# Kernel optimization log

Hardware: AMD Instinct MI355X
Metric: run time of the kernel (lower is better)

Reference implementation:

```python
import jax, jax.numpy as jnp
import numpy as np
from jax import lax

NIMG = 4          # num_image_channels (dx for these is zeroed each step)
C = 64            # total channels = 4 + 44 + 16
NFILT = 2         # learned depthwise filters
HID = 256         # hidden_size
FIRE = 0.5        # fire_rate
B, H, W = 16, 128, 128
STEPS = 8


def setup_inputs() -> dict:
    key = jax.random.key(0)
    ks = jax.random.split(key, 7)
    x = jax.random.normal(ks[0], (B, H, W, C), jnp.float32)
    # depthwise 3x3 kernels, OIHW with I=1 (groups = C)
    w_conv1 = jax.random.normal(ks[1], (C, 1, 3, 3), jnp.float32) * 0.3
    w_conv2 = jax.random.normal(ks[2], (C, 1, 3, 3), jnp.float32) * 0.3
    fan_in = C * (NFILT + 1)  # 192
    w_hidden = jax.random.normal(ks[3], (HID, fan_in), jnp.float32) / np.sqrt(fan_in).astype(np.float32)
    b_hidden = jax.random.normal(ks[4], (HID,), jnp.float32) * 0.01
    # original zero-inits final_layer; use small random weights for a nontrivial baseline
    w_final = jax.random.normal(ks[5], (C, HID), jnp.float32) * 0.02
    rand_vals = jax.random.uniform(ks[6], (STEPS, B, H, W, 1), jnp.float32)
    return {"x": x, "w_conv1": w_conv1, "w_conv2": w_conv2,
            "w_hidden": w_hidden, "b_hidden": b_hidden, "w_final": w_final,
            "rand_vals": rand_vals, "steps": STEPS}


def _dwconv(xc, w):
    # xc: [B, C, W, H]; reflect-pad then valid depthwise 3x3 (groups=C)
    xp = jnp.pad(xc, ((0, 0), (0, 0), (1, 1), (1, 1)), mode='reflect')
    return lax.conv_general_dilated(xp, w, (1, 1), 'VALID',
                                    dimension_numbers=('NCHW', 'OIHW', 'NCHW'),
                                    feature_group_count=C)


def reference(x, w_conv1, w_conv2, w_hidden, b_hidden, w_final, rand_vals, steps):
    dtype = x.dtype
    ch_mask = (jnp.arange(C) >= NIMG).astype(dtype)  # zero image-channel updates

    def step(xc, rnd):
        # xc: [B, C, W, H]  (torch layout after x.transpose(1,3))
        y = jnp.concatenate([xc, _dwconv(xc, w_conv1), _dwconv(xc, w_conv2)], axis=1)  # [B,3C,W,H]
        yt = jnp.transpose(y, (0, 3, 2, 1))  # [B,H,W,3C]
        h = jax.nn.relu(jnp.einsum('bhwf,of->bhwo', yt, w_hidden) + b_hidden)
        dx = jnp.einsum('bhwo,co->bhwc', h, w_final)  # [B,H,W,C]
        dx = dx * (rnd > FIRE).astype(dtype) * ch_mask  # stochastic gate + immutable image channels
        xc = xc + jnp.transpose(dx, (0, 3, 2, 1))
        life = (xc[:, 0:1] > 0).astype(dtype)  # channel-0 life mask broadcast over channels
        return xc * life, None

    xc0 = jnp.transpose(x, (0, 3, 2, 1))  # NHWC -> [B,C,W,H]
    xcN, _ = lax.scan(step, xc0, rand_vals)
    return jnp.transpose(xcN, (0, 3, 2, 1))  # back to NHWC
```

## Files before the change

kernel.cpp:

```cpp
#include <hip/hip_runtime.h>

#define BB 16
#define HH 128
#define WW 128
#define CH 64
#define TPX 64
#define NTH 512
#define NPIX (BB*HH*WW)
#define KF 192
#define HID 256

#define WS_WTP 0u
#define WS_WFP 98304u
#define WS_WCB 131072u
#define WS_ST  135680u

typedef __attribute__((ext_vector_type(8))) short short8;
typedef __attribute__((ext_vector_type(8))) unsigned short ushort8;
typedef __attribute__((ext_vector_type(4))) float f4;

#define OFF_WCV 25344
#define OFF_FC  32768
#define OFF_LG  49152
#define SMEM_SZ 49664

#define GLDS16(gp, lp) __builtin_amdgcn_global_load_lds( \
    (const __attribute__((address_space(1))) unsigned int*)(gp), \
    (__attribute__((address_space(3))) unsigned int*)(lp), 16, 0, 0)

__device__ __forceinline__ unsigned short f2b(float f) {
    unsigned x = __float_as_uint(f);
    x += 0x7fffu + ((x >> 16) & 1u);
    return (unsigned short)(x >> 16);
}
__device__ __forceinline__ float b2f(unsigned short u) {
    return __uint_as_float(((unsigned)u) << 16);
}
__device__ __forceinline__ int refl(int i, int n) {
    if (i < 0) return -i;
    if (i >= n) return 2*n - 2 - i;
    return i;
}
__device__ __forceinline__ int xrow(int row, int chunk) {
    return row*64 + (((chunk ^ row) & 7) << 3);
}

__global__ __launch_bounds__(256) void prep(
    const float* __restrict__ wh, const float* __restrict__ wf,
    unsigned short* __restrict__ wtp, unsigned short* __restrict__ wfp)
{
    int i = blockIdx.x * 256 + threadIdx.x;
    if (i < 6144) {
        const int l = i & 63, r = i >> 6;
        const int ks = r % 6, ti = r / 6;
        const int row = ti*16 + (l & 15);
        const int k0  = ks*32 + (l >> 4)*8;
        ushort8 v;
        #pragma unroll
        for (int j = 0; j < 8; ++j) v[j] = f2b(wh[row*KF + k0 + j]);
        *(ushort8*)&wtp[(size_t)i * 8] = v;
    } else {
        const int g = i - 6144;
        const int l = g & 63, r = g >> 6;
        const int ks2 = r & 7, cq = r >> 3;
        const int c  = cq*16 + (l & 15);
        const int o0 = ks2*32 + (l >> 4)*8;
        ushort8 v;
        #pragma unroll
        for (int j = 0; j < 8; ++j) v[j] = f2b(wf[c*HID + o0 + j]);
        *(ushort8*)&wfp[(size_t)g * 8] = v;
    }
}

__global__ __launch_bounds__(256) void prep2(
    const float* __restrict__ w1, const float* __restrict__ w2,
    float* __restrict__ wcb)
{
    int i = blockIdx.x * 256 + threadIdx.x;
    if (i < 1152) {
        const int f = i / 576, rem = i - f * 576;
        const int t = rem >> 6, c = rem & 63;
        wcb[i] = (f ? w2 : w1)[c*9 + t];
    }
}

template<int SRCF, int DSTF>
__global__ __launch_bounds__(512, 4) void nca_step(
    const float* __restrict__ xinf, const unsigned short* __restrict__ srcb,
    void* __restrict__ dstv,
    const unsigned short* __restrict__ wtp, const unsigned short* __restrict__ wfp,
    const float* __restrict__ wcbg,
    const float* __restrict__ bh, const float* __restrict__ rnd)
{
    __shared__ __align__(16) char smem[SMEM_SZ];
    unsigned short* xs   = (unsigned short*)smem;
    char*           fch  = smem + OFF_FC;
    float*          wcvb = (float*)(smem + OFF_WCV);
    float*          lgs  = (float*)(smem + OFF_LG);

    const int tid = threadIdx.x;
    const int l = tid & 63, wv = tid >> 6;
    const int lr = l & 15, gq = l >> 4;
    const int w0 = blockIdx.x * TPX;
    const int h  = blockIdx.y;
    const int b  = blockIdx.z;
    const int R  = b * HH + h;

    if (SRCF == 1) {
        #pragma unroll
        for (int it = 0; it < 3; ++it) {
            const int g = wv + it*8;
            const int c = g*64 + l;
            const int row = c >> 3, ckp = c & 7;
            const int r3 = row / 66, px = row - r3*66;
            const int ck = ckp ^ (row & 7);
            const int sr = refl(h - 1 + r3, HH);
            const int sc = refl(w0 - 1 + px, WW);
            const unsigned short* gp = srcb + ((((size_t)b*HH + sr)*WW + sc) << 6) + (ck << 3);
            GLDS16(gp, (char*)xs + (size_t)g*1024);
        }
        if (wv == 0 && l < 48) {
            const int c = 1536 + l;
            const int row = c >> 3, ckp = c & 7;
            const int r3 = row / 66, px = row - r3*66;
            const int ck = ckp ^ (row & 7);
            const int sr = refl(h - 1 + r3, HH);
            const int sc = refl(w0 - 1 + px, WW);
            const unsigned short* gp = srcb + ((((size_t)b*HH + sr)*WW + sc) << 6) + (ck << 3);
            GLDS16(gp, (char*)xs + (size_t)24*1024);
        }
    } else {
        const int q = tid & 3;
        for (int s0 = tid >> 2; s0 < 198; s0 += 128) {
            const int r3 = s0 / 66, wi = s0 - r3*66;
            const int sr = refl(h - 1 + r3, HH);
            const int sc = refl(w0 - 1 + wi, WW);
            const size_t pix = ((size_t)b*HH + sr)*WW + sc;
            const float* p = xinf + pix*64 + q*16;
            f4 a0 = *(const f4*)p, a1 = *(const f4*)(p+4);
            f4 a2 = *(const f4*)(p+8), a3 = *(const f4*)(p+12);
            ushort8 o0, o1;
            o0[0]=f2b(a0.x); o0[1]=f2b(a0.y); o0[2]=f2b(a0.z); o0[3]=f2b(a0.w);
            o0[4]=f2b(a1.x); o0[5]=f2b(a1.y); o0[6]=f2b(a1.z); o0[7]=f2b(a1.w);
            o1[0]=f2b(a2.x); o1[1]=f2b(a2.y); o1[2]=f2b(a2.z); o1[3]=f2b(a2.w);
            o1[4]=f2b(a3.x); o1[5]=f2b(a3.y); o1[6]=f2b(a3.z); o1[7]=f2b(a3.w);
            const int row = r3*66 + wi;
            *(ushort8*)(xs + xrow(row, 2*q))     = o0;
            *(ushort8*)(xs + xrow(row, 2*q + 1)) = o1;
        }
    }
    for (int j = tid; j < 288; j += NTH)
        ((f4*)wcvb)[j] = ((const f4*)wcbg)[j];
    if (tid < TPX) {
        const size_t pix = (size_t)R * WW + w0 + tid;
        lgs[TPX + tid] = (rnd[pix] > 0.5f) ? 1.f : 0.f;
        if (SRCF == 0)
            lgs[tid] = (xinf[pix*64] > 0.f) ? 1.f : 0.f;
    }
    __syncthreads();

    if (SRCF == 1 && tid < TPX)
        lgs[tid] = (b2f(xs[xrow(66 + tid + 1, 0)]) > 0.f) ? 1.f : 0.f;

    {
        const int px = tid >> 3, ck = tid & 7, cg = ck * 8;
        float a1[8], a2[8];
        #pragma unroll
        for (int k = 0; k < 8; ++k) { a1[k] = 0.f; a2[k] = 0.f; }
        #pragma unroll
        for (int t = 0; t < 9; ++t) {
            const int i2 = t / 3, j = t - 3*i2;
            const ushort8 xv = *(const ushort8*)(xs + xrow(j*66 + px + i2, ck));
            const float* w1p = wcvb + t*64 + cg;
            const float* w2p = wcvb + 576 + t*64 + cg;
            #pragma unroll
            for (int k = 0; k < 8; ++k) {
                const float xf = b2f(xv[k]);
                a1[k] = fmaf(xf, w1p[k], a1[k]);
                a2[k] = fmaf(xf, w2p[k], a2[k]);
            }
        }
        ushort8 o1v, o2v;
        #pragma unroll
        for (int k = 0; k < 8; ++k) { o1v[k] = f2b(a1[k]); o2v[k] = f2b(a2[k]); }
        const int sw = (px & 7) << 4;
        *(ushort8*)(fch + ((px*256 + cg*2) ^ sw))       = o1v;
        *(ushort8*)(fch + ((px*256 + 128 + cg*2) ^ sw)) = o2v;
    }
    __syncthreads();

    f4 acc[4][2];
    #pragma unroll
    for (int ot = 0; ot < 2; ++ot) {
        const float bv = bh[wv*32 + ot*16 + lr];
        const f4 bvv = {bv, bv, bv, bv};
        #pragma unroll
        for (int mt = 0; mt < 4; ++mt) acc[mt][ot] = bvv;
    }
    #pragma unroll
    for (int ks = 0; ks < 6; ++ks) {
        short8 afr[4];
        #pragma unroll
        for (int mt = 0; mt < 4; ++mt) {
            const int px = mt*16 + lr;
            if (ks < 2)
                afr[mt] = *(const short8*)(xs + xrow(66 + px + 1, ks*4 + gq));
            else
                afr[mt] = *(const short8*)(fch +
                            ((px*256 + (ks-2)*64 + gq*16) ^ ((px & 7) << 4)));
        }
        #pragma unroll
        for (int ot = 0; ot < 2; ++ot) {
            const short8 bfr = *(const short8*)(wtp + ((((wv*2 + ot)*6 + ks)*64 + l) << 3));
            #pragma unroll
            for (int mt = 0; mt < 4; ++mt)
                acc[mt][ot] = __builtin_amdgcn_mfma_f32_16x16x32_bf16(afr[mt], bfr, acc[mt][ot], 0,0,0);
        }
    }

    const int cq = wv & 3, mh = wv >> 2;
    unsigned short baseb[8];
    #pragma unroll
    for (int mt = 0; mt < 2; ++mt)
      #pragma unroll
      for (int r2 = 0; r2 < 4; ++r2) {
        const int px = mh*32 + mt*16 + gq*4 + r2;
        baseb[mt*4 + r2] = xs[xrow(66 + px + 1, cq*2 + (lr >> 3)) + (lr & 7)];
      }
    __syncthreads();

    #pragma unroll
    for (int mt = 0; mt < 4; ++mt)
      #pragma unroll
      for (int ot = 0; ot < 2; ++ot)
        #pragma unroll
        for (int r2 = 0; r2 < 4; ++r2) {
            const int px = mt*16 + gq*4 + r2;
            const int o  = wv*32 + ot*16 + lr;
            *(unsigned short*)(smem + ((px*512 + o*2) ^ ((px & 7) << 4))) =
                f2b(fmaxf(acc[mt][ot][r2], 0.f));
        }
    __syncthreads();

    f4 acc2[2] = {{0.f,0.f,0.f,0.f},{0.f,0.f,0.f,0.f}};
    #pragma unroll
    for (int ks2 = 0; ks2 < 8; ++ks2) {
        const short8 bw = *(const short8*)(wfp + (((cq*8 + ks2)*64 + l) << 3));
        #pragma unroll
        for (int mt = 0; mt < 2; ++mt) {
            const int px = mh*32 + mt*16 + lr;
            const short8 ha = *(const short8*)(smem + ((px*512 + ks2*64 + gq*16) ^ ((px & 7) << 4)));
            acc2[mt] = __builtin_amdgcn_mfma_f32_16x16x32_bf16(ha, bw, acc2[mt], 0,0,0);
        }
    }

    unsigned short* stageB = (unsigned short*)fch;
    float*          stageF = (float*)fch;
    #pragma unroll
    for (int mt = 0; mt < 2; ++mt)
      #pragma unroll
      for (int r2 = 0; r2 < 4; ++r2) {
        const int px = mh*32 + mt*16 + gq*4 + r2;
        const int c  = cq*16 + lr;
        const float life = lgs[px], g = lgs[TPX + px];
        const float base = b2f(baseb[mt*4 + r2]);
        const float dx   = acc2[mt][r2];
        const float outv = (c >= 4) ? (base + dx * g) * life : base * life;
        if (DSTF == 1) stageF[px*64 + c] = outv;
        else           stageB[px*64 + c] = f2b(outv);
      }
    __syncthreads();

    const size_t pix0 = (size_t)R * WW + w0;
    if (DSTF == 1) {
        float* dstf = (float*)dstv + pix0 * 64;
        for (int i = tid; i < 1024; i += NTH) {
            const f4 v = *(const f4*)(stageF + i*4);
            __builtin_nontemporal_store(v, (f4*)(dstf + i*4));
        }
    } else {
        unsigned short* dstb = (unsigned short*)dstv + pix0 * 64;
        const ushort8 v = *(const ushort8*)(stageB + tid*8);
        __builtin_nontemporal_store(v, (ushort8*)(dstb + tid*8));
    }
}

extern "C" void kernel_launch(void* const* d_in, const int* in_sizes, int n_in,
                              void* d_out, int out_size, void* d_ws, size_t ws_size,
                              hipStream_t stream) {
    const float* xin = (const float*)d_in[0];
    const float* w1  = (const float*)d_in[1];
    const float* w2  = (const float*)d_in[2];
    const float* wh  = (const float*)d_in[3];
    const float* bh  = (const float*)d_in[4];
    const float* wf  = (const float*)d_in[5];
    const float* rv  = (const float*)d_in[6];

    unsigned short* wtp = (unsigned short*)((char*)d_ws + WS_WTP);
    unsigned short* wfp = (unsigned short*)((char*)d_ws + WS_WFP);
    float*          wcb = (float*)((char*)d_ws + WS_WCB);
    unsigned short* stb = (unsigned short*)((char*)d_ws + WS_ST);
    unsigned short* omb = (unsigned short*)d_out;

    prep <<<dim3(32), dim3(256), 0, stream>>>(wh, wf, wtp, wfp);
    prep2<<<dim3(5),  dim3(256), 0, stream>>>(w1, w2, wcb);

    dim3 g(WW / TPX, HH, BB), blk(NTH);
    nca_step<0,0><<<g, blk, 0, stream>>>(xin, nullptr, stb, wtp, wfp, wcb, bh, rv);
    for (int s = 1; s < 7; ++s) {
        const unsigned short* sp = (s & 1) ? stb : omb;
        unsigned short* dp       = (s & 1) ? omb : stb;
        nca_step<1,0><<<g, blk, 0, stream>>>(nullptr, sp, dp, wtp, wfp, wcb, bh,
                                             rv + (size_t)s * NPIX);
    }
    nca_step<1,1><<<g, blk, 0, stream>>>(nullptr, stb, d_out, wtp, wfp, wcb, bh,
                                         rv + (size_t)7 * NPIX);
}
```

Before: 634.0 us.

## Fold depthwise convolutions into hidden-layer weights as a 576-wide MFMA GEMM

Precomputes combined weights W_hidden·conv1/conv2 per 3x3 tap (plus identity at center) so the hidden layer becomes a single K=576 bf16 MFMA GEMM over the 9 shifted neighborhood rows. This removes the scalar FMA depthwise convolution stage, its LDS staging buffer and a barrier. The trade is three times more MFMA work and larger weight fetches from global memory. Precision also shifts, since the fused weights are rounded to bf16 and the conv outputs are never rounded separately.

```diff
diff --git a/kernel.cpp b/kernel.cpp
--- a/kernel.cpp
+++ b/kernel.cpp
@@ -7,20 +7,18 @@
 #define TPX 64
 #define NTH 512
 #define NPIX (BB*HH*WW)
-#define KF 192
+#define KFT 576
 #define HID 256
 
 #define WS_WTP 0u
-#define WS_WFP 98304u
-#define WS_WCB 131072u
-#define WS_ST  135680u
+#define WS_WFP 294912u
+#define WS_ST  327680u
 
 typedef __attribute__((ext_vector_type(8))) short short8;
 typedef __attribute__((ext_vector_type(8))) unsigned short ushort8;
 typedef __attribute__((ext_vector_type(4))) float f4;
 
-#define OFF_WCV 25344
-#define OFF_FC  32768
+#define OFF_STG 32768
 #define OFF_LG  49152
 #define SMEM_SZ 49664
 
@@ -47,20 +45,28 @@
 
 __global__ __launch_bounds__(256) void prep(
     const float* __restrict__ wh, const float* __restrict__ wf,
+    const float* __restrict__ w1, const float* __restrict__ w2,
     unsigned short* __restrict__ wtp, unsigned short* __restrict__ wfp)
 {
     int i = blockIdx.x * 256 + threadIdx.x;
-    if (i < 6144) {
+    if (i < 18432) {
         const int l = i & 63, r = i >> 6;
-        const int ks = r % 6, ti = r / 6;
-        const int row = ti*16 + (l & 15);
-        const int k0  = ks*32 + (l >> 4)*8;
+        const int ks = r % 18, ti = r / 18;
+        const int o  = ti*16 + (l & 15);
+        const int k0 = ks*32 + (l >> 4)*8;
         ushort8 v;
         #pragma unroll
-        for (int j = 0; j < 8; ++j) v[j] = f2b(wh[row*KF + k0 + j]);
+        for (int j = 0; j < 8; ++j) {
+            const int k = k0 + j;
+            const int t = k >> 6, c = k & 63;
+            float val = wh[o*192 + 64 + c]  * w1[c*9 + t]
+                      + wh[o*192 + 128 + c] * w2[c*9 + t];
+            if (t == 4) val += wh[o*192 + c];
+            v[j] = f2b(val);
+        }
         *(ushort8*)&wtp[(size_t)i * 8] = v;
-    } else {
-        const int g = i - 6144;
+    } else if (i < 20480) {
+        const int g = i - 18432;
         const int l = g & 63, r = g >> 6;
         const int ks2 = r & 7, cq = r >> 3;
         const int c  = cq*16 + (l & 15);
@@ -72,31 +78,17 @@
     }
 }
 
-__global__ __launch_bounds__(256) void prep2(
-    const float* __restrict__ w1, const float* __restrict__ w2,
-    float* __restrict__ wcb)
-{
-    int i = blockIdx.x * 256 + threadIdx.x;
-    if (i < 1152) {
-        const int f = i / 576, rem = i - f * 576;
-        const int t = rem >> 6, c = rem & 63;
-        wcb[i] = (f ? w2 : w1)[c*9 + t];
-    }
-}
-
 template<int SRCF, int DSTF>
 __global__ __launch_bounds__(512, 4) void nca_step(
     const float* __restrict__ xinf, const unsigned short* __restrict__ srcb,
     void* __restrict__ dstv,
     const unsigned short* __restrict__ wtp, const unsigned short* __restrict__ wfp,
-    const float* __restrict__ wcbg,
     const float* __restrict__ bh, const float* __restrict__ rnd)
 {
     __shared__ __align__(16) char smem[SMEM_SZ];
-    unsigned short* xs   = (unsigned short*)smem;
-    char*           fch  = smem + OFF_FC;
-    float*          wcvb = (float*)(smem + OFF_WCV);
-    float*          lgs  = (float*)(smem + OFF_LG);
+    unsigned short* xs  = (unsigned short*)smem;
+    char*           stg = smem + OFF_STG;
+    float*          lgs = (float*)(smem + OFF_LG);
 
     const int tid = threadIdx.x;
     const int l = tid & 63, wv = tid >> 6;
@@ -149,8 +141,6 @@
             *(ushort8*)(xs + xrow(row, 2*q + 1)) = o1;
         }
     }
-    for (int j = tid; j < 288; j += NTH)
-        ((f4*)wcvb)[j] = ((const f4*)wcbg)[j];
     if (tid < TPX) {
         const size_t pix = (size_t)R * WW + w0 + tid;
         lgs[TPX + tid] = (rnd[pix] > 0.5f) ? 1.f : 0.f;
@@ -162,33 +152,6 @@
     if (SRCF == 1 && tid < TPX)
         lgs[tid] = (b2f(xs[xrow(66 + tid + 1, 0)]) > 0.f) ? 1.f : 0.f;
 
-    {
-        const int px = tid >> 3, ck = tid & 7, cg = ck * 8;
-        float a1[8], a2[8];
-        #pragma unroll
-        for (int k = 0; k < 8; ++k) { a1[k] = 0.f; a2[k] = 0.f; }
-        #pragma unroll
-        for (int t = 0; t < 9; ++t) {
-            const int i2 = t / 3, j = t - 3*i2;
-            const ushort8 xv = *(const ushort8*)(xs + xrow(j*66 + px + i2, ck));
-            const float* w1p = wcvb + t*64 + cg;
-            const float* w2p = wcvb + 576 + t*64 + cg;
-            #pragma unroll
-            for (int k = 0; k < 8; ++k) {
-                const float xf = b2f(xv[k]);
-                a1[k] = fmaf(xf, w1p[k], a1[k]);
-                a2[k] = fmaf(xf, w2p[k], a2[k]);
-            }
-        }
-        ushort8 o1v, o2v;
-        #pragma unroll
-        for (int k = 0; k < 8; ++k) { o1v[k] = f2b(a1[k]); o2v[k] = f2b(a2[k]); }
-        const int sw = (px & 7) << 4;
-        *(ushort8*)(fch + ((px*256 + cg*2) ^ sw))       = o1v;
-        *(ushort8*)(fch + ((px*256 + 128 + cg*2) ^ sw)) = o2v;
-    }
-    __syncthreads();
-
     f4 acc[4][2];
     #pragma unroll
     for (int ot = 0; ot < 2; ++ot) {
@@ -198,20 +161,18 @@
         for (int mt = 0; mt < 4; ++mt) acc[mt][ot] = bvv;
     }
     #pragma unroll
-    for (int ks = 0; ks < 6; ++ks) {
+    for (int ks = 0; ks < 18; ++ks) {
+        const int t = ks >> 1, half = ks & 1;
+        const int i2 = t / 3, j = t - 3*i2;
         short8 afr[4];
         #pragma unroll
         for (int mt = 0; mt < 4; ++mt) {
             const int px = mt*16 + lr;
-            if (ks < 2)
-                afr[mt] = *(const short8*)(xs + xrow(66 + px + 1, ks*4 + gq));
-            else
-                afr[mt] = *(const short8*)(fch +
-                            ((px*256 + (ks-2)*64 + gq*16) ^ ((px & 7) << 4)));
+            afr[mt] = *(const short8*)(xs + xrow(j*66 + px + i2, half*4 + gq));
         }
         #pragma unroll
         for (int ot = 0; ot < 2; ++ot) {
-            const short8 bfr = *(const short8*)(wtp + ((((wv*2 + ot)*6 + ks)*64 + l) << 3));
+            const short8 bfr = *(const short8*)(wtp + ((((wv*2 + ot)*18 + ks)*64 + l) << 3));
             #pragma unroll
             for (int mt = 0; mt < 4; ++mt)
                 acc[mt][ot] = __builtin_amdgcn_mfma_f32_16x16x32_bf16(afr[mt], bfr, acc[mt][ot], 0,0,0);
@@ -254,8 +215,8 @@
         }
     }
 
-    unsigned short* stageB = (unsigned short*)fch;
-    float*          stageF = (float*)fch;
+    unsigned short* stageB = (unsigned short*)stg;
+    float*          stageF = (float*)stg;
     #pragma unroll
     for (int mt = 0; mt < 2; ++mt)
       #pragma unroll
@@ -298,21 +259,19 @@
 
     unsigned short* wtp = (unsigned short*)((char*)d_ws + WS_WTP);
     unsigned short* wfp = (unsigned short*)((char*)d_ws + WS_WFP);
-    float*          wcb = (float*)((char*)d_ws + WS_WCB);
     unsigned short* stb = (unsigned short*)((char*)d_ws + WS_ST);
     unsigned short* omb = (unsigned short*)d_out;
 
-    prep <<<dim3(32), dim3(256), 0, stream>>>(wh, wf, wtp, wfp);
-    prep2<<<dim3(5),  dim3(256), 0, stream>>>(w1, w2, wcb);
+    prep<<<dim3(80), dim3(256), 0, stream>>>(wh, wf, w1, w2, wtp, wfp);
 
     dim3 g(WW / TPX, HH, BB), blk(NTH);
-    nca_step<0,0><<<g, blk, 0, stream>>>(xin, nullptr, stb, wtp, wfp, wcb, bh, rv);
+    nca_step<0,0><<<g, blk, 0, stream>>>(xin, nullptr, stb, wtp, wfp, bh, rv);
     for (int s = 1; s < 7; ++s) {
         const unsigned short* sp = (s & 1) ? stb : omb;
         unsigned short* dp       = (s & 1) ? omb : stb;
-        nca_step<1,0><<<g, blk, 0, stream>>>(nullptr, sp, dp, wtp, wfp, wcb, bh,
+        nca_step<1,0><<<g, blk, 0, stream>>>(nullptr, sp, dp, wtp, wfp, bh,
                                              rv + (size_t)s * NPIX);
     }
-    nca_step<1,1><<<g, blk, 0, stream>>>(nullptr, stb, d_out, wtp, wfp, wcb, bh,
+    nca_step<1,1><<<g, blk, 0, stream>>>(nullptr, stb, d_out, wtp, wfp, bh,
                                          rv + (size_t)7 * NPIX);
 }
```

Result: slower. 747.3 us (+17.9%).

## Halve per-block pixel tile to 32 with 256 threads and remap wave work split

Applied to the files above, without the earlier changes.

Shrinks each block from 64 to 32 pixels per row segment with 4 waves instead of 8, and resizes the shared-memory layout to about 26 KB. Each wave now computes 64 hidden units for both 16-pixel tiles in the first GEMM, and 16 pixels by 32 channels in the second. A separate staging area is added for the output. The aim is higher occupancy and more blocks per CU. The cost is a larger halo overhead, since 34 columns are loaded per 32 output pixels, and more weight-fragment reloads per pixel.

```diff
diff --git a/kernel.cpp b/kernel.cpp
--- a/kernel.cpp
+++ b/kernel.cpp
@@ -4,8 +4,8 @@
 #define HH 128
 #define WW 128
 #define CH 64
-#define TPX 64
-#define NTH 512
+#define TPX 32
+#define NTH 256
 #define NPIX (BB*HH*WW)
 #define KF 192
 #define HID 256
@@ -19,10 +19,11 @@
 typedef __attribute__((ext_vector_type(8))) unsigned short ushort8;
 typedef __attribute__((ext_vector_type(4))) float f4;
 
-#define OFF_WCV 25344
-#define OFF_FC  32768
-#define OFF_LG  49152
-#define SMEM_SZ 49664
+#define OFF_FC  13056
+#define OFF_STG 16384
+#define OFF_WCV 21248
+#define OFF_LG  25856
+#define SMEM_SZ 26112
 
 #define GLDS16(gp, lp) __builtin_amdgcn_global_load_lds( \
     (const __attribute__((address_space(1))) unsigned int*)(gp), \
@@ -85,7 +86,7 @@
 }
 
 template<int SRCF, int DSTF>
-__global__ __launch_bounds__(512, 4) void nca_step(
+__global__ __launch_bounds__(256, 4) void nca_step(
     const float* __restrict__ xinf, const unsigned short* __restrict__ srcb,
     void* __restrict__ dstv,
     const unsigned short* __restrict__ wtp, const unsigned short* __restrict__ wfp,
@@ -95,6 +96,7 @@
     __shared__ __align__(16) char smem[SMEM_SZ];
     unsigned short* xs   = (unsigned short*)smem;
     char*           fch  = smem + OFF_FC;
+    char*           stg  = smem + OFF_STG;
     float*          wcvb = (float*)(smem + OFF_WCV);
     float*          lgs  = (float*)(smem + OFF_LG);
 
@@ -109,10 +111,10 @@
     if (SRCF == 1) {
         #pragma unroll
         for (int it = 0; it < 3; ++it) {
-            const int g = wv + it*8;
+            const int g = wv + it*4;
             const int c = g*64 + l;
             const int row = c >> 3, ckp = c & 7;
-            const int r3 = row / 66, px = row - r3*66;
+            const int r3 = row / 34, px = row - r3*34;
             const int ck = ckp ^ (row & 7);
             const int sr = refl(h - 1 + r3, HH);
             const int sc = refl(w0 - 1 + px, WW);
@@ -120,19 +122,19 @@
             GLDS16(gp, (char*)xs + (size_t)g*1024);
         }
         if (wv == 0 && l < 48) {
-            const int c = 1536 + l;
+            const int c = 768 + l;
             const int row = c >> 3, ckp = c & 7;
-            const int r3 = row / 66, px = row - r3*66;
+            const int r3 = row / 34, px = row - r3*34;
             const int ck = ckp ^ (row & 7);
             const int sr = refl(h - 1 + r3, HH);
             const int sc = refl(w0 - 1 + px, WW);
             const unsigned short* gp = srcb + ((((size_t)b*HH + sr)*WW + sc) << 6) + (ck << 3);
-            GLDS16(gp, (char*)xs + (size_t)24*1024);
+            GLDS16(gp, (char*)xs + (size_t)12*1024);
         }
     } else {
         const int q = tid & 3;
-        for (int s0 = tid >> 2; s0 < 198; s0 += 128) {
-            const int r3 = s0 / 66, wi = s0 - r3*66;
+        for (int s0 = tid >> 2; s0 < 102; s0 += 64) {
+            const int r3 = s0 / 34, wi = s0 - r3*34;
             const int sr = refl(h - 1 + r3, HH);
             const int sc = refl(w0 - 1 + wi, WW);
             const size_t pix = ((size_t)b*HH + sr)*WW + sc;
@@ -144,7 +146,7 @@
             o0[4]=f2b(a1.x); o0[5]=f2b(a1.y); o0[6]=f2b(a1.z); o0[7]=f2b(a1.w);
             o1[0]=f2b(a2.x); o1[1]=f2b(a2.y); o1[2]=f2b(a2.z); o1[3]=f2b(a2.w);
             o1[4]=f2b(a3.x); o1[5]=f2b(a3.y); o1[6]=f2b(a3.z); o1[7]=f2b(a3.w);
-            const int row = r3*66 + wi;
+            const int row = r3*34 + wi;
             *(ushort8*)(xs + xrow(row, 2*q))     = o0;
             *(ushort8*)(xs + xrow(row, 2*q + 1)) = o1;
         }
@@ -160,7 +162,7 @@
     __syncthreads();
 
     if (SRCF == 1 && tid < TPX)
-        lgs[tid] = (b2f(xs[xrow(66 + tid + 1, 0)]) > 0.f) ? 1.f : 0.f;
+        lgs[tid] = (b2f(xs[xrow(34 + tid + 1, 0)]) > 0.f) ? 1.f : 0.f;
 
     {
         const int px = tid >> 3, ck = tid & 7, cg = ck * 8;
@@ -170,7 +172,7 @@
         #pragma unroll
         for (int t = 0; t < 9; ++t) {
             const int i2 = t / 3, j = t - 3*i2;
-            const ushort8 xv = *(const ushort8*)(xs + xrow(j*66 + px + i2, ck));
+            const ushort8 xv = *(const ushort8*)(xs + xrow(j*34 + px + i2, ck));
             const float* w1p = wcvb + t*64 + cg;
             const float* w2p = wcvb + 576 + t*64 + cg;
             #pragma unroll
@@ -189,54 +191,53 @@
     }
     __syncthreads();
 
-    f4 acc[4][2];
-    #pragma unroll
-    for (int ot = 0; ot < 2; ++ot) {
-        const float bv = bh[wv*32 + ot*16 + lr];
+    f4 acc[2][4];
+    #pragma unroll
+    for (int ot = 0; ot < 4; ++ot) {
+        const float bv = bh[wv*64 + ot*16 + lr];
         const f4 bvv = {bv, bv, bv, bv};
-        #pragma unroll
-        for (int mt = 0; mt < 4; ++mt) acc[mt][ot] = bvv;
+        acc[0][ot] = bvv; acc[1][ot] = bvv;
     }
     #pragma unroll
     for (int ks = 0; ks < 6; ++ks) {
-        short8 afr[4];
-        #pragma unroll
-        for (int mt = 0; mt < 4; ++mt) {
+        short8 afr[2];
+        #pragma unroll
+        for (int mt = 0; mt < 2; ++mt) {
             const int px = mt*16 + lr;
             if (ks < 2)
-                afr[mt] = *(const short8*)(xs + xrow(66 + px + 1, ks*4 + gq));
+                afr[mt] = *(const short8*)(xs + xrow(34 + px + 1, ks*4 + gq));
             else
                 afr[mt] = *(const short8*)(fch +
                             ((px*256 + (ks-2)*64 + gq*16) ^ ((px & 7) << 4)));
         }
         #pragma unroll
-        for (int ot = 0; ot < 2; ++ot) {
-            const short8 bfr = *(const short8*)(wtp + ((((wv*2 + ot)*6 + ks)*64 + l) << 3));
-            #pragma unroll
-            for (int mt = 0; mt < 4; ++mt)
-                acc[mt][ot] = __builtin_amdgcn_mfma_f32_16x16x32_bf16(afr[mt], bfr, acc[mt][ot], 0,0,0);
-        }
-    }
-
-    const int cq = wv & 3, mh = wv >> 2;
+        for (int ot = 0; ot < 4; ++ot) {
+            const short8 bfr = *(const short8*)(wtp + ((((wv*4 + ot)*6 + ks)*64 + l) << 3));
+            acc[0][ot] = __builtin_amdgcn_mfma_f32_16x16x32_bf16(afr[0], bfr, acc[0][ot], 0,0,0);
+            acc[1][ot] = __builtin_amdgcn_mfma_f32_16x16x32_bf16(afr[1], bfr, acc[1][ot], 0,0,0);
+        }
+    }
+
+    const int mh = wv >> 1, cs = wv & 1;
     unsigned short baseb[8];
+    #pragma unroll
+    for (int ct = 0; ct < 2; ++ct)
+      #pragma unroll
+      for (int r2 = 0; r2 < 4; ++r2) {
+        const int px = mh*16 + gq*4 + r2;
+        const int c  = cs*32 + ct*16 + lr;
+        baseb[ct*4 + r2] = xs[xrow(34 + px + 1, c >> 3) + (c & 7)];
+      }
+    __syncthreads();
+
     #pragma unroll
     for (int mt = 0; mt < 2; ++mt)
       #pragma unroll
-      for (int r2 = 0; r2 < 4; ++r2) {
-        const int px = mh*32 + mt*16 + gq*4 + r2;
-        baseb[mt*4 + r2] = xs[xrow(66 + px + 1, cq*2 + (lr >> 3)) + (lr & 7)];
-      }
-    __syncthreads();
-
-    #pragma unroll
-    for (int mt = 0; mt < 4; ++mt)
-      #pragma unroll
-      for (int ot = 0; ot < 2; ++ot)
+      for (int ot = 0; ot < 4; ++ot)
         #pragma unroll
         for (int r2 = 0; r2 < 4; ++r2) {
             const int px = mt*16 + gq*4 + r2;
-            const int o  = wv*32 + ot*16 + lr;
+            const int o  = wv*64 + ot*16 + lr;
             *(unsigned short*)(smem + ((px*512 + o*2) ^ ((px & 7) << 4))) =
                 f2b(fmaxf(acc[mt][ot][r2], 0.f));
         }
@@ -245,26 +246,26 @@
     f4 acc2[2] = {{0.f,0.f,0.f,0.f},{0.f,0.f,0.f,0.f}};
     #pragma unroll
     for (int ks2 = 0; ks2 < 8; ++ks2) {
-        const short8 bw = *(const short8*)(wfp + (((cq*8 + ks2)*64 + l) << 3));
-        #pragma unroll
-        for (int mt = 0; mt < 2; ++mt) {
-            const int px = mh*32 + mt*16 + lr;
-            const short8 ha = *(const short8*)(smem + ((px*512 + ks2*64 + gq*16) ^ ((px & 7) << 4)));
-            acc2[mt] = __builtin_amdgcn_mfma_f32_16x16x32_bf16(ha, bw, acc2[mt], 0,0,0);
-        }
-    }
-
-    unsigned short* stageB = (unsigned short*)fch;
-    float*          stageF = (float*)fch;
-    #pragma unroll
-    for (int mt = 0; mt < 2; ++mt)
+        const int px = mh*16 + lr;
+        const short8 ha = *(const short8*)(smem + ((px*512 + ks2*64 + gq*16) ^ ((px & 7) << 4)));
+        #pragma unroll
+        for (int ct = 0; ct < 2; ++ct) {
+            const short8 bw = *(const short8*)(wfp + ((((cs*2 + ct)*8 + ks2)*64 + l) << 3));
+            acc2[ct] = __builtin_amdgcn_mfma_f32_16x16x32_bf16(ha, bw, acc2[ct], 0,0,0);
+        }
+    }
+
+    unsigned short* stageB = (unsigned short*)stg;
+    float*          stageF = (float*)stg;
+    #pragma unroll
+    for (int ct = 0; ct < 2; ++ct)
       #pragma unroll
       for (int r2 = 0; r2 < 4; ++r2) {
-        const int px = mh*32 + mt*16 + gq*4 + r2;
-        const int c  = cq*16 + lr;
+        const int px = mh*16 + gq*4 + r2;
+        const int c  = cs*32 + ct*16 + lr;
         const float life = lgs[px], g = lgs[TPX + px];
-        const float base = b2f(baseb[mt*4 + r2]);
-        const float dx   = acc2[mt][r2];
+        const float base = b2f(baseb[ct*4 + r2]);
+        const float dx   = acc2[ct][r2];
         const float outv = (c >= 4) ? (base + dx * g) * life : base * life;
         if (DSTF == 1) stageF[px*64 + c] = outv;
         else           stageB[px*64 + c] = f2b(outv);
@@ -274,7 +275,7 @@
     const size_t pix0 = (size_t)R * WW + w0;
     if (DSTF == 1) {
         float* dstf = (float*)dstv + pix0 * 64;
-        for (int i = tid; i < 1024; i += NTH) {
+        for (int i = tid; i < 512; i += NTH) {
             const f4 v = *(const f4*)(stageF + i*4);
             __builtin_nontemporal_store(v, (f4*)(dstf + i*4));
         }
```

New measurement: 610.0 us. 3.8% less time.
